# Optimization experiments

Hardware: AMD Instinct MI355X
Metric: run time of the kernel (lower is better)

## Reference

```python
import jax, jax.numpy as jnp
import numpy as np

B, C, D, H, W = 4096, 128, 9, 8, 8  # batch, in_dims, d_emb, fmap_size, fmap_size
EPS = 1e-10


def setup_inputs() -> dict:
    key = jax.random.key(0)
    k1, k2 = jax.random.split(key)
    fcn_activations = jax.random.normal(k1, (B, C, H, W), dtype=jnp.float32)
    # precomputed spatial kernel buffer (emb2 in the torch module): [1, out_dims, H, W]
    emb2 = jax.random.normal(k2, (1, C * D, H, W), dtype=jnp.float32)
    return {"fcn_activations": fcn_activations, "emb2": emb2}


def reference(fcn_activations, emb2):
    b, c, h, w = fcn_activations.shape
    d = emb2.shape[1] // c  # d_emb
    # idx1 = arange(c*d)//d, i.e. channel i is repeated d times consecutively.
    # gather + elementwise mult + spatial sum == contraction below (no big emb1 intermediate):
    kern = emb2.reshape(c, d, h, w)
    out = jnp.einsum('bchw,cdhw->bcd', fcn_activations, kern).reshape(b, c * d)
    # L2Norm over last dim
    norm = jnp.sqrt(jnp.sum(out * out, axis=-1) + EPS)
    return out / norm[:, None]
```

## Files before the change

kernel.cpp:

```cpp
#include <hip/hip_runtime.h>


constexpr int B_TOT  = 4096;
constexpr int C_CH   = 128;
constexpr int D_EMB  = 9;
constexpr int THREADS = 256;
constexpr int GPB    = 32;
constexpr int RB     = 16;
constexpr int CHK    = 8;

__global__ __launch_bounds__(THREADS, 3)
void esenc_main(const float* __restrict__ fcn,
                const float* __restrict__ kern,
                float* __restrict__ out,
                float* __restrict__ partial) {
    __shared__ float red[THREADS];
    const int tid = threadIdx.x;
    const int l   = tid & 7;
    const int g   = tid >> 3;
    const int ct  = blockIdx.x & 3;
    const int bt  = blockIdx.x >> 2;
    const int c   = ct * GPB + g;
    const int b0  = bt * RB;

    const float4* kern4 = (const float4*)kern;
    const float4* f4    = (const float4*)fcn;

    float4 k0[D_EMB], k1[D_EMB];
#pragma unroll
    for (int d = 0; d < D_EMB; ++d) {
        const size_t kb = (size_t)(c * D_EMB + d) * 16;
        k0[d] = kern4[kb + l];
        k1[d] = kern4[kb + 8 + l];
    }

#pragma unroll
    for (int chk = 0; chk < RB / CHK; ++chk) {
        const int bb = b0 + chk * CHK;

        size_t fb = ((size_t)bb * C_CH + c) * 16;
        float4 a0 = f4[fb + l];
        float4 a1 = f4[fb + 8 + l];

        float keep[D_EMB];
#pragma unroll
        for (int d = 0; d < D_EMB; ++d) keep[d] = 0.0f;

#pragma unroll
        for (int r = 0; r < CHK; ++r) {
            const float4 c0 = a0, c1 = a1;
            if (r + 1 < CHK) {
                const size_t fn = ((size_t)(bb + r + 1) * C_CH + c) * 16;
                a0 = f4[fn + l];
                a1 = f4[fn + 8 + l];
            }
            float p[D_EMB];
#pragma unroll
            for (int d = 0; d < D_EMB; ++d) {
                float t;
                t = c0.x * k0[d].x;
                t = fmaf(c0.y, k0[d].y, t);
                t = fmaf(c0.z, k0[d].z, t);
                t = fmaf(c0.w, k0[d].w, t);
                t = fmaf(c1.x, k1[d].x, t);
                t = fmaf(c1.y, k1[d].y, t);
                t = fmaf(c1.z, k1[d].z, t);
                t = fmaf(c1.w, k1[d].w, t);
                p[d] = t;
            }
#pragma unroll
            for (int m = 1; m < 8; m <<= 1) {
#pragma unroll
                for (int d = 0; d < D_EMB; ++d)
                    p[d] += __shfl_xor(p[d], m, 8);
            }
            if (l == r) {
#pragma unroll
                for (int d = 0; d < D_EMB; ++d) keep[d] = p[d];
            }
        }

        float* op = out + (size_t)(bb + l) * (C_CH * D_EMB) + c * D_EMB;
        float s = 0.0f;
#pragma unroll
        for (int d = 0; d < D_EMB; ++d) {
            op[d] = keep[d];
            s = fmaf(keep[d], keep[d], s);
        }

        if (chk) __syncthreads();
        red[tid] = s;
        __syncthreads();
        if (tid < CHK) {
            float t = 0.0f;
#pragma unroll
            for (int gg = 0; gg < GPB; ++gg) t += red[gg * 8 + tid];
            partial[ct * B_TOT + bb + tid] = t;
        }
    }
}

__global__ __launch_bounds__(256)
void esenc_norm(float* __restrict__ out, const float* __restrict__ partial) {
    constexpr int ROW4 = C_CH * D_EMB / 4;
    constexpr int N4   = B_TOT * ROW4;
    float4* o4 = (float4*)out;
    for (int i = blockIdx.x * blockDim.x + threadIdx.x; i < N4;
         i += gridDim.x * blockDim.x) {
        const int b = i / ROW4;
        const float s = partial[b] + partial[B_TOT + b] +
                        partial[2 * B_TOT + b] + partial[3 * B_TOT + b];
        const float inv = 1.0f / sqrtf(s + 1e-10f);
        float4 v = o4[i];
        v.x *= inv; v.y *= inv; v.z *= inv; v.w *= inv;
        o4[i] = v;
    }
}

extern "C" void kernel_launch(void* const* d_in, const int* in_sizes, int n_in,
                              void* d_out, int out_size, void* d_ws, size_t ws_size,
                              hipStream_t stream) {
    const float* fcn  = (const float*)d_in[0];
    const float* kern = (const float*)d_in[1];
    float* out = (float*)d_out;
    float* partial = (float*)d_ws;

    dim3 grid1((B_TOT / RB) * (C_CH / GPB)), block1(THREADS);
    hipLaunchKernelGGL(esenc_main, grid1, block1, 0, stream, fcn, kern, out, partial);

    dim3 grid2(2048), block2(256);
    hipLaunchKernelGGL(esenc_norm, grid2, block2, 0, stream, out, partial);
}
```

Baseline: 37.16 us.

## Fuse L2 normalization into main kernel by giving each block all channels

Measured after the change: 36.80 us. Within noise of the previous version (-1.0%).

```diff
diff --git a/kernel.cpp b/kernel.cpp
--- a/kernel.cpp
+++ b/kernel.cpp
@@ -1,56 +1,53 @@
 #include <hip/hip_runtime.h>
 
 
-constexpr int B_TOT  = 4096;
-constexpr int C_CH   = 128;
-constexpr int D_EMB  = 9;
+constexpr int B_TOT = 4096;
+constexpr int C_CH  = 128;
+constexpr int D_EMB = 9;
 constexpr int THREADS = 256;
-constexpr int GPB    = 32;
-constexpr int RB     = 16;
-constexpr int CHK    = 8;
+constexpr int GPB = 32;
+constexpr int NCH = 4;
+constexpr int RB  = 8;
 
-__global__ __launch_bounds__(THREADS, 3)
-void esenc_main(const float* __restrict__ fcn,
-                const float* __restrict__ kern,
-                float* __restrict__ out,
-                float* __restrict__ partial) {
-    __shared__ float red[THREADS];
+__global__ __launch_bounds__(THREADS)
+void esenc_fused(const float* __restrict__ fcn,
+                 const float* __restrict__ kern,
+                 float* __restrict__ out) {
+    __shared__ float red[4 * RB];
+    __shared__ float invn[RB];
+
     const int tid = threadIdx.x;
     const int l   = tid & 7;
     const int g   = tid >> 3;
-    const int ct  = blockIdx.x & 3;
-    const int bt  = blockIdx.x >> 2;
-    const int c   = ct * GPB + g;
-    const int b0  = bt * RB;
+    const int w   = tid >> 6;
+    const int b0  = blockIdx.x * RB;
 
     const float4* kern4 = (const float4*)kern;
     const float4* f4    = (const float4*)fcn;
 
-    float4 k0[D_EMB], k1[D_EMB];
-#pragma unroll
-    for (int d = 0; d < D_EMB; ++d) {
-        const size_t kb = (size_t)(c * D_EMB + d) * 16;
-        k0[d] = kern4[kb + l];
-        k1[d] = kern4[kb + 8 + l];
-    }
+    float keep[NCH][D_EMB];
 
 #pragma unroll
-    for (int chk = 0; chk < RB / CHK; ++chk) {
-        const int bb = b0 + chk * CHK;
+    for (int ch = 0; ch < NCH; ++ch) {
+        const int c = ch * GPB + g;
 
-        size_t fb = ((size_t)bb * C_CH + c) * 16;
+        float4 k0[D_EMB], k1[D_EMB];
+#pragma unroll
+        for (int d = 0; d < D_EMB; ++d) {
+            const size_t kb = (size_t)(c * D_EMB + d) * 16;
+            k0[d] = kern4[kb + l];
+            k1[d] = kern4[kb + 8 + l];
+        }
+
+        const size_t fb = ((size_t)b0 * C_CH + c) * 16;
         float4 a0 = f4[fb + l];
         float4 a1 = f4[fb + 8 + l];
 
-        float keep[D_EMB];
 #pragma unroll
-        for (int d = 0; d < D_EMB; ++d) keep[d] = 0.0f;
-
-#pragma unroll
-        for (int r = 0; r < CHK; ++r) {
+        for (int r = 0; r < RB; ++r) {
             const float4 c0 = a0, c1 = a1;
-            if (r + 1 < CHK) {
-                const size_t fn = ((size_t)(bb + r + 1) * C_CH + c) * 16;
+            if (r + 1 < RB) {
+                const size_t fn = ((size_t)(b0 + r + 1) * C_CH + c) * 16;
                 a0 = f4[fn + l];
                 a1 = f4[fn + 8 + l];
             }
@@ -76,44 +73,37 @@
             }
             if (l == r) {
 #pragma unroll
-                for (int d = 0; d < D_EMB; ++d) keep[d] = p[d];
+                for (int d = 0; d < D_EMB; ++d) keep[ch][d] = p[d];
             }
         }
+    }
 
-        float* op = out + (size_t)(bb + l) * (C_CH * D_EMB) + c * D_EMB;
-        float s = 0.0f;
+    float s = 0.0f;
 #pragma unroll
-        for (int d = 0; d < D_EMB; ++d) {
-            op[d] = keep[d];
-            s = fmaf(keep[d], keep[d], s);
-        }
+    for (int ch = 0; ch < NCH; ++ch)
+#pragma unroll
+        for (int d = 0; d < D_EMB; ++d)
+            s = fmaf(keep[ch][d], keep[ch][d], s);
 
-        if (chk) __syncthreads();
-        red[tid] = s;
-        __syncthreads();
-        if (tid < CHK) {
-            float t = 0.0f;
+    s += __shfl_xor(s, 8,  64);
+    s += __shfl_xor(s, 16, 64);
+    s += __shfl_xor(s, 32, 64);
+    if ((tid & 63) < 8) red[w * RB + l] = s;
+    __syncthreads();
+    if (tid < RB) {
+        const float t = red[tid] + red[RB + tid] + red[2 * RB + tid] + red[3 * RB + tid];
+        invn[tid] = 1.0f / sqrtf(t + 1e-10f);
+    }
+    __syncthreads();
+    const float inv = invn[l];
+
 #pragma unroll
-            for (int gg = 0; gg < GPB; ++gg) t += red[gg * 8 + tid];
-            partial[ct * B_TOT + bb + tid] = t;
-        }
-    }
-}
-
-__global__ __launch_bounds__(256)
-void esenc_norm(float* __restrict__ out, const float* __restrict__ partial) {
-    constexpr int ROW4 = C_CH * D_EMB / 4;
-    constexpr int N4   = B_TOT * ROW4;
-    float4* o4 = (float4*)out;
-    for (int i = blockIdx.x * blockDim.x + threadIdx.x; i < N4;
-         i += gridDim.x * blockDim.x) {
-        const int b = i / ROW4;
-        const float s = partial[b] + partial[B_TOT + b] +
-                        partial[2 * B_TOT + b] + partial[3 * B_TOT + b];
-        const float inv = 1.0f / sqrtf(s + 1e-10f);
-        float4 v = o4[i];
-        v.x *= inv; v.y *= inv; v.z *= inv; v.w *= inv;
-        o4[i] = v;
+    for (int ch = 0; ch < NCH; ++ch) {
+        const int c = ch * GPB + g;
+        float* op = out + (size_t)(b0 + l) * (C_CH * D_EMB) + c * D_EMB;
+#pragma unroll
+        for (int d = 0; d < D_EMB; ++d)
+            op[d] = keep[ch][d] * inv;
     }
 }
 
@@ -123,11 +113,7 @@
     const float* fcn  = (const float*)d_in[0];
     const float* kern = (const float*)d_in[1];
     float* out = (float*)d_out;
-    float* partial = (float*)d_ws;
 
-    dim3 grid1((B_TOT / RB) * (C_CH / GPB)), block1(THREADS);
-    hipLaunchKernelGGL(esenc_main, grid1, block1, 0, stream, fcn, kern, out, partial);
-
-    dim3 grid2(2048), block2(256);
-    hipLaunchKernelGGL(esenc_norm, grid2, block2, 0, stream, out, partial);
+    dim3 grid(B_TOT / RB), block(THREADS);
+    hipLaunchKernelGGL(esenc_fused, grid, block, 0, stream, fcn, kern, out);
 }
```

## Use DPP row reductions, drop manual prefetch, raise occupancy hint

Applied to the files above, without the earlier changes.

Result: slower. 85.95 us (+131.3%).

```diff
diff --git a/kernel.cpp b/kernel.cpp
--- a/kernel.cpp
+++ b/kernel.cpp
@@ -1,27 +1,35 @@
 #include <hip/hip_runtime.h>
 
 
-constexpr int B_TOT  = 4096;
-constexpr int C_CH   = 128;
-constexpr int D_EMB  = 9;
+constexpr int B_TOT = 4096;
+constexpr int C_CH  = 128;
+constexpr int D_EMB = 9;
 constexpr int THREADS = 256;
-constexpr int GPB    = 32;
-constexpr int RB     = 16;
-constexpr int CHK    = 8;
+constexpr int GPB = 32;
+constexpr int RB  = 16;
+constexpr int CHK = 8;
 
-__global__ __launch_bounds__(THREADS, 3)
+__device__ __forceinline__ float reduce8_hw(float p) {
+    p += __int_as_float(__builtin_amdgcn_mov_dpp(__float_as_int(p), 0xB1,  0xf, 0xf, true));
+    p += __int_as_float(__builtin_amdgcn_mov_dpp(__float_as_int(p), 0x4E,  0xf, 0xf, true));
+    p += __int_as_float(__builtin_amdgcn_mov_dpp(__float_as_int(p), 0x141, 0xf, 0xf, true));
+    return p;
+}
+
+__global__ __launch_bounds__(THREADS, 4)
 void esenc_main(const float* __restrict__ fcn,
                 const float* __restrict__ kern,
                 float* __restrict__ out,
                 float* __restrict__ partial) {
     __shared__ float red[THREADS];
+
     const int tid = threadIdx.x;
     const int l   = tid & 7;
     const int g   = tid >> 3;
     const int ct  = blockIdx.x & 3;
     const int bt  = blockIdx.x >> 2;
-    const int c   = ct * GPB + g;
-    const int b0  = bt * RB;
+    const unsigned b0 = (unsigned)bt * RB;
+    const unsigned c  = (unsigned)(ct * GPB + g);
 
     const float4* kern4 = (const float4*)kern;
     const float4* f4    = (const float4*)fcn;
@@ -29,54 +37,34 @@
     float4 k0[D_EMB], k1[D_EMB];
 #pragma unroll
     for (int d = 0; d < D_EMB; ++d) {
-        const size_t kb = (size_t)(c * D_EMB + d) * 16;
+        const unsigned kb = (c * D_EMB + (unsigned)d) * 16u;
         k0[d] = kern4[kb + l];
-        k1[d] = kern4[kb + 8 + l];
+        k1[d] = kern4[kb + 8u + l];
     }
 
 #pragma unroll
     for (int chk = 0; chk < RB / CHK; ++chk) {
-        const int bb = b0 + chk * CHK;
-
-        size_t fb = ((size_t)bb * C_CH + c) * 16;
-        float4 a0 = f4[fb + l];
-        float4 a1 = f4[fb + 8 + l];
-
+        const unsigned bb = b0 + (unsigned)(chk * CHK);
         float keep[D_EMB];
-#pragma unroll
-        for (int d = 0; d < D_EMB; ++d) keep[d] = 0.0f;
 
 #pragma unroll
         for (int r = 0; r < CHK; ++r) {
-            const float4 c0 = a0, c1 = a1;
-            if (r + 1 < CHK) {
-                const size_t fn = ((size_t)(bb + r + 1) * C_CH + c) * 16;
-                a0 = f4[fn + l];
-                a1 = f4[fn + 8 + l];
-            }
-            float p[D_EMB];
+            const unsigned fb = ((bb + (unsigned)r) * C_CH + c) * 16u;
+            const float4 a0 = f4[fb + l];
+            const float4 a1 = f4[fb + 8u + l];
 #pragma unroll
             for (int d = 0; d < D_EMB; ++d) {
                 float t;
-                t = c0.x * k0[d].x;
-                t = fmaf(c0.y, k0[d].y, t);
-                t = fmaf(c0.z, k0[d].z, t);
-                t = fmaf(c0.w, k0[d].w, t);
-                t = fmaf(c1.x, k1[d].x, t);
-                t = fmaf(c1.y, k1[d].y, t);
-                t = fmaf(c1.z, k1[d].z, t);
-                t = fmaf(c1.w, k1[d].w, t);
-                p[d] = t;
-            }
-#pragma unroll
-            for (int m = 1; m < 8; m <<= 1) {
-#pragma unroll
-                for (int d = 0; d < D_EMB; ++d)
-                    p[d] += __shfl_xor(p[d], m, 8);
-            }
-            if (l == r) {
-#pragma unroll
-                for (int d = 0; d < D_EMB; ++d) keep[d] = p[d];
+                t = a0.x * k0[d].x;
+                t = fmaf(a0.y, k0[d].y, t);
+                t = fmaf(a0.z, k0[d].z, t);
+                t = fmaf(a0.w, k0[d].w, t);
+                t = fmaf(a1.x, k1[d].x, t);
+                t = fmaf(a1.y, k1[d].y, t);
+                t = fmaf(a1.z, k1[d].z, t);
+                t = fmaf(a1.w, k1[d].w, t);
+                t = reduce8_hw(t);
+                if (l == r) keep[d] = t;
             }
         }
 
@@ -95,7 +83,7 @@
             float t = 0.0f;
 #pragma unroll
             for (int gg = 0; gg < GPB; ++gg) t += red[gg * 8 + tid];
-            partial[ct * B_TOT + bb + tid] = t;
+            partial[ct * B_TOT + (int)bb + tid] = t;
         }
     }
 }
@@ -125,9 +113,9 @@
     float* out = (float*)d_out;
     float* partial = (float*)d_ws;
 
-    dim3 grid1((B_TOT / RB) * (C_CH / GPB)), block1(THREADS);
+    dim3 grid1((B_TOT / RB) * 4), block1(THREADS);
     hipLaunchKernelGGL(esenc_main, grid1, block1, 0, stream, fcn, kern, out, partial);
 
-    dim3 grid2(2048), block2(256);
+    dim3 grid2(1024), block2(256);
     hipLaunchKernelGGL(esenc_norm, grid2, block2, 0, stream, out, partial);
 }
```
